# Kernel optimization log

Measured on AMD Instinct MI355X. Metric: run time of the kernel, lower is better.

Reference implementation:

```python
import jax, jax.numpy as jnp
import numpy as np

N_NODES = 50000
N_EDGES = 500000
N_GRAPHS = 256
D_IN, D_H1, D_H2, D_H3, D_OUT = 768, 256, 128, 64, 2


def _glorot(key, shape):
    fan_in, fan_out = shape[1], shape[0]
    lim = float(np.sqrt(6.0 / (fan_in + fan_out)))
    return jax.random.uniform(key, shape, jnp.float32, -lim, lim)


def setup_inputs() -> dict:
    key = jax.random.key(0)
    ks = jax.random.split(key, 12)
    x = jax.random.normal(ks[0], (N_NODES, D_IN), jnp.float32)
    edge_index = jax.random.randint(ks[1], (2, N_EDGES), 0, N_NODES, jnp.int64)
    batch = jnp.sort(jax.random.randint(ks[2], (N_NODES,), 0, N_GRAPHS, jnp.int64))
    return {
        "x": x,
        "edge_index": edge_index,
        "batch": batch,
        # SAGEConv1: out = lin_l(mean_aggr) + lin_r(x); bias only on lin_l (PyG default)
        "W1_l": _glorot(ks[3], (D_H1, D_IN)),
        "b1_l": jnp.zeros((D_H1,), jnp.float32),
        "W1_r": _glorot(ks[4], (D_H1, D_IN)),
        # SAGEConv2
        "W2_l": _glorot(ks[5], (D_H2, D_H1)),
        "b2_l": jnp.zeros((D_H2,), jnp.float32),
        "W2_r": _glorot(ks[6], (D_H2, D_H1)),
        # MLP head
        "W3": _glorot(ks[7], (D_H3, D_H2)),
        "b3": jnp.zeros((D_H3,), jnp.float32),
        "W4": _glorot(ks[8], (D_OUT, D_H3)),
        "b4": jnp.zeros((D_OUT,), jnp.float32),
    }


def _sage_conv(x, src, dst, deg_inv, W_l, b_l, W_r):
    # mean aggregation of neighbor features: scatter-add then divide by in-degree
    aggr = jax.ops.segment_sum(x[src], dst, num_segments=N_NODES)  # [N, d]
    aggr = aggr * deg_inv[:, None]
    return aggr @ W_l.T + b_l + x @ W_r.T


def reference(x, edge_index, batch, W1_l, b1_l, W1_r, W2_l, b2_l, W2_r, W3, b3, W4, b4):
    src, dst = edge_index[0], edge_index[1]
    deg = jax.ops.segment_sum(jnp.ones((N_EDGES,), x.dtype), dst, num_segments=N_NODES)
    deg_inv = jnp.where(deg > 0, 1.0 / jnp.maximum(deg, 1.0), 0.0)

    h = jax.nn.relu(_sage_conv(x, src, dst, deg_inv, W1_l, b1_l, W1_r))
    h = jax.nn.relu(_sage_conv(h, src, dst, deg_inv, W2_l, b2_l, W2_r))

    # global_mean_pool over graph ids
    pooled = jax.ops.segment_sum(h, batch, num_segments=N_GRAPHS)  # [G, 128]
    cnt = jax.ops.segment_sum(jnp.ones((N_NODES,), h.dtype), batch, num_segments=N_GRAPHS)
    pooled = pooled / jnp.maximum(cnt, 1.0)[:, None]

    # dropout is identity in eval mode
    h = pooled @ W3.T + b3
    h = h @ W4.T + b4
    return jax.nn.softmax(h, axis=-1)
```

## Files before the change

### kernel.cpp

```cpp
#include <hip/hip_runtime.h>
#include <cstdint>
#include <cstddef>

#define N_NODES 50000
#define N_EDGES 500000
#define N_GRAPHS 256
#define D_IN 768
#define D_H1 256
#define D_H2 128

typedef __attribute__((ext_vector_type(8))) __bf16 bf16x8;
typedef __attribute__((ext_vector_type(4))) float f32x4;

__device__ __forceinline__ float bf2f(uint32_t u) {
    union { uint32_t i; float f; } v; v.i = u << 16; return v.f;
}
__device__ __forceinline__ uint32_t f2bf(float f) {
    union { float f; uint32_t i; } v; v.f = f;
    uint32_t u = v.i;
    return (u + 0x7FFFu + ((u >> 16) & 1u)) >> 16;
}

#define HIST4_BLKS 489
#define PACKA4_BLKS 4688
#define PACKW1_BLKS 192
#define PACKW2_BLKS 32
#define NCHUNK_A 4800000
__global__ __launch_bounds__(256) void k_pack_hist(
    const float* __restrict__ x, uint16_t* __restrict__ xp,
    const float* __restrict__ W1l, const float* __restrict__ W1r, uint16_t* __restrict__ W1p,
    const float* __restrict__ W2l, const float* __restrict__ W2r, uint16_t* __restrict__ W2p,
    const int* __restrict__ e_dst, int* __restrict__ deg)
{
    int b = blockIdx.x, t = threadIdx.x;
    if (b < HIST4_BLKS) {
        int base = b * 1024 + t;
        #pragma unroll
        for (int j = 0; j < 4; ++j) {
            int e = base + j * 256;
            if (e < N_EDGES) atomicAdd(&deg[e_dst[e]], 1);
        }
    } else if (b < HIST4_BLKS + PACKA4_BLKS) {
        int c0 = (b - HIST4_BLKS) * 1024 + t;
        float4 u[4], v[4];
        #pragma unroll
        for (int j = 0; j < 4; ++j) {
            int c = c0 + j * 256; if (c > NCHUNK_A - 1) c = NCHUNK_A - 1;
            int l = c & 63, tt = c >> 6;
            int kt = tt % 24, mt = tt / 24;
            const float* p = x + (size_t)(mt * 16 + (l & 15)) * 768 + kt * 32 + (l >> 4) * 8;
            u[j] = *(const float4*)p;
            v[j] = *(const float4*)(p + 4);
        }
        #pragma unroll
        for (int j = 0; j < 4; ++j) {
            int c = c0 + j * 256; if (c > NCHUNK_A - 1) c = NCHUNK_A - 1;
            uint4 o;
            o.x = f2bf(u[j].x) | (f2bf(u[j].y) << 16);
            o.y = f2bf(u[j].z) | (f2bf(u[j].w) << 16);
            o.z = f2bf(v[j].x) | (f2bf(v[j].y) << 16);
            o.w = f2bf(v[j].z) | (f2bf(v[j].w) << 16);
            *(uint4*)(xp + (size_t)c * 8) = o;
        }
    } else if (b < HIST4_BLKS + PACKA4_BLKS + PACKW1_BLKS) {
        int c = (b - HIST4_BLKS - PACKA4_BLKS) * 256 + t;
        int l = c & 63, tt = c >> 6;
        int kt = tt % 24, mt = tt / 24;
        int row = mt * 16 + (l & 15);
        const float* src = (row < 256) ? (W1l + (size_t)row * 768)
                                       : (W1r + (size_t)(row - 256) * 768);
        const float* p = src + kt * 32 + (l >> 4) * 8;
        float4 u = *(const float4*)p, v = *(const float4*)(p + 4);
        uint4 o;
        o.x = f2bf(u.x) | (f2bf(u.y) << 16);
        o.y = f2bf(u.z) | (f2bf(u.w) << 16);
        o.z = f2bf(v.x) | (f2bf(v.y) << 16);
        o.w = f2bf(v.z) | (f2bf(v.w) << 16);
        *(uint4*)(W1p + (size_t)c * 8) = o;
    } else {
        int c = (b - HIST4_BLKS - PACKA4_BLKS - PACKW1_BLKS) * 256 + t;
        int l = c & 63, tt = c >> 6;
        int kt = tt % 8, mt = tt / 8;
        int row = mt * 16 + (l & 15);
        const float* src = (row < 128) ? (W2l + (size_t)row * 256)
                                       : (W2r + (size_t)(row - 128) * 256);
        const float* p = src + kt * 32 + (l >> 4) * 8;
        float4 u = *(const float4*)p, v = *(const float4*)(p + 4);
        uint4 o;
        o.x = f2bf(u.x) | (f2bf(u.y) << 16);
        o.y = f2bf(u.z) | (f2bf(u.w) << 16);
        o.z = f2bf(v.x) | (f2bf(v.y) << 16);
        o.w = f2bf(v.z) | (f2bf(v.w) << 16);
        *(uint4*)(W2p + (size_t)c * 8) = o;
    }
}

#define SCAN_BLKS 196
#define G1_OFF  SCAN_BLKS
#define G1_BLKS 784
#define FILL_OFF (G1_OFF + G1_BLKS)
#define FILL_BLKS 1954
__global__ __launch_bounds__(256, 2) void k_scan_gemm1_fill(
    const uint16_t* __restrict__ Ap, const uint16_t* __restrict__ Bp,
    uint16_t* __restrict__ Cl, uint16_t* __restrict__ Cr,
    const int* __restrict__ e_src, const int* __restrict__ e_dst,
    const int* __restrict__ deg, int* __restrict__ row_start,
    int* __restrict__ cursor, float* __restrict__ deg_inv,
    int* __restrict__ bsum, int* __restrict__ scan_done,
    int* __restrict__ csr_src)
{
    int t = threadIdx.x;
    if (blockIdx.x < SCAN_BLKS) {
        __shared__ int buf[256];
        __shared__ int bbuf[256];
        int b = blockIdx.x, i = b * 256 + t;
        int v = (i < N_NODES) ? deg[i] : 0;
        buf[t] = v; __syncthreads();
        for (int off = 1; off < 256; off <<= 1) {
            int u = (t >= off) ? buf[t - off] : 0;
            __syncthreads(); buf[t] += u; __syncthreads();
        }
        if (t == 255) atomicExch(&bsum[b], buf[255] + 1);
        int w = 0;
        if (t < SCAN_BLKS) {
            do { w = atomicAdd(&bsum[t], 0); } while (w == 0);
            w -= 1;
        }
        bbuf[t] = w; __syncthreads();
        for (int off = 1; off < 256; off <<= 1) {
            int u = (t >= off) ? bbuf[t - off] : 0;
            __syncthreads(); bbuf[t] += u; __syncthreads();
        }
        int base = (b > 0) ? bbuf[b - 1] : 0;
        if (i < N_NODES) {
            int rs = base + buf[t] - v;
            row_start[i] = rs;
            cursor[i] = rs;
            deg_inv[i] = (v > 0) ? (1.0f / (float)v) : 0.0f;
        }
        if (b == 0 && t == 0) row_start[N_NODES] = N_EDGES;
        __threadfence();
        __syncthreads();
        if (t == 0)
            __hip_atomic_fetch_add(scan_done, 1, __ATOMIC_RELEASE, __HIP_MEMORY_SCOPE_AGENT);
        return;
    }
    if (blockIdx.x >= FILL_OFF) {
        if (t < 64) {
            while (__hip_atomic_load(scan_done, __ATOMIC_ACQUIRE,
                                     __HIP_MEMORY_SCOPE_AGENT) < SCAN_BLKS)
                __builtin_amdgcn_s_sleep(8);
        }
        __syncthreads();
        int e = (blockIdx.x - FILL_OFF) * 256 + t;
        if (e < N_EDGES) {
            int d = e_dst[e];
            int pos = atomicAdd(&cursor[d], 1);
            csr_src[pos] = e_src[e];
        }
        return;
    }
    const int i = blockIdx.x - G1_OFF;
    const int pr = (i >> 4) * 8 + (i & 7);
    const int half = (i >> 3) & 1;
    if (pr >= 391) return;
    const int KT = 24;
    const int wave = t >> 6, lane = t & 63;
    const int fr = lane & 15, fq = lane >> 4;
    const int bm = pr * 128;
    const int wm = (wave >> 1) * 64, wn = (wave & 1) * 128;
    const int mtiles = (N_NODES + 15) >> 4;

    const bf16x8* ap[4];
    const bf16x8* bp[8];
    #pragma unroll
    for (int mi = 0; mi < 4; ++mi) {
        int mt = ((bm + wm) >> 4) + mi;
        if (mt > mtiles - 1) mt = mtiles - 1;
        ap[mi] = (const bf16x8*)Ap + (size_t)mt * KT * 64 + lane;
    }
    #pragma unroll
    for (int ni = 0; ni < 8; ++ni) {
        int nt = ((half * 256 + wn) >> 4) + ni;
        bp[ni] = (const bf16x8*)Bp + (size_t)nt * KT * 64 + lane;
    }

    f32x4 acc[4][8] = {};
    bf16x8 a0[4], b0[8], a1[4], b1[8];

    auto lA = [&](int kt, bf16x8* d) {
        #pragma unroll
        for (int mi = 0; mi < 4; ++mi) d[mi] = ap[mi][kt * 64];
    };
    auto lB = [&](int kt, bf16x8* d) {
        #pragma unroll
        for (int ni = 0; ni < 8; ++ni) d[ni] = bp[ni][kt * 64];
    };
    auto step = [&](bf16x8* a, bf16x8* b) {
        #pragma unroll
        for (int mi = 0; mi < 4; ++mi)
            #pragma unroll
            for (int ni = 0; ni < 8; ++ni)
                acc[mi][ni] = __builtin_amdgcn_mfma_f32_16x16x32_bf16(
                    a[mi], b[ni], acc[mi][ni], 0, 0, 0);
    };

    lA(0, a0); lB(0, b0);
    for (int ks = 0; ks < KT; ks += 2) {
        lA(ks + 1, a1); lB(ks + 1, b1);
        step(a0, b0);
        if (ks + 2 < KT) { lA(ks + 2, a0); lB(ks + 2, b0); }
        step(a1, b1);
    }

    uint16_t* __restrict__ C = half ? Cr : Cl;
    #pragma unroll
    for (int mi = 0; mi < 4; ++mi) {
        #pragma unroll
        for (int r = 0; r < 4; ++r) {
            int row = bm + wm + mi * 16 + fq * 4 + r;
            if (row >= N_NODES) continue;
            #pragma unroll
            for (int ni = 0; ni < 8; ++ni) {
                int col = wn + ni * 16 + fr;
                C[(size_t)row * 256 + col] = (uint16_t)f2bf(acc[mi][ni][r]);
            }
        }
    }
}

__global__ __launch_bounds__(256, 2) void k_mgemm(
    const uint16_t* __restrict__ Ap, const uint16_t* __restrict__ Bp,
    uint16_t* __restrict__ C, int M, int N, int KT)
{
    const int tid = threadIdx.x;
    const int wave = tid >> 6, lane = tid & 63;
    const int fr = lane & 15, fq = lane >> 4;
    const int bn = blockIdx.x * 256, bm = blockIdx.y * 128;
    const int wm = (wave >> 1) * 64, wn = (wave & 1) * 128;
    const int mtiles = (M + 15) >> 4;

    const bf16x8* ap[4];
    const bf16x8* bp[8];
    #pragma unroll
    for (int mi = 0; mi < 4; ++mi) {
        int mt = ((bm + wm) >> 4) + mi;
        if (mt > mtiles - 1) mt = mtiles - 1;
        ap[mi] = (const bf16x8*)Ap + (size_t)mt * KT * 64 + lane;
    }
    #pragma unroll
    for (int ni = 0; ni < 8; ++ni) {
        int nt = ((bn + wn) >> 4) + ni;
        bp[ni] = (const bf16x8*)Bp + (size_t)nt * KT * 64 + lane;
    }

    f32x4 acc[4][8] = {};
    bf16x8 a0[4], b0[8], a1[4], b1[8];

    auto lA = [&](int kt, bf16x8* d) {
        #pragma unroll
        for (int mi = 0; mi < 4; ++mi) d[mi] = ap[mi][kt * 64];
    };
    auto lB = [&](int kt, bf16x8* d) {
        #pragma unroll
        for (int ni = 0; ni < 8; ++ni) d[ni] = bp[ni][kt * 64];
    };
    auto step = [&](bf16x8* a, bf16x8* b) {
        #pragma unroll
        for (int mi = 0; mi < 4; ++mi)
            #pragma unroll
            for (int ni = 0; ni < 8; ++ni)
                acc[mi][ni] = __builtin_amdgcn_mfma_f32_16x16x32_bf16(
                    a[mi], b[ni], acc[mi][ni], 0, 0, 0);
    };

    lA(0, a0); lB(0, b0);
    for (int ks = 0; ks < KT; ks += 2) {
        lA(ks + 1, a1); lB(ks + 1, b1);
        step(a0, b0);
        if (ks + 2 < KT) { lA(ks + 2, a0); lB(ks + 2, b0); }
        step(a1, b1);
    }

    #pragma unroll
    for (int mi = 0; mi < 4; ++mi) {
        #pragma unroll
        for (int r = 0; r < 4; ++r) {
            int row = bm + wm + mi * 16 + fq * 4 + r;
            if (row >= M) continue;
            #pragma unroll
            for (int ni = 0; ni < 8; ++ni) {
                int col = bn + wn + ni * 16 + fr;
                C[(size_t)row * N + col] = (uint16_t)f2bf(acc[mi][ni][r]);
            }
        }
    }
}

__global__ __launch_bounds__(256) void k_agg1(
    const uint16_t* __restrict__ yl, const uint16_t* __restrict__ yr,
    const int* __restrict__ row_start, const int* __restrict__ csr,
    const float* __restrict__ deg_inv, const float* __restrict__ bias,
    uint16_t* __restrict__ h1p)
{
    int node = blockIdx.x * 8 + (threadIdx.x >> 5);
    if (node >= N_NODES) return;
    int c = threadIdx.x & 31;
    int s = row_start[node], e = row_start[node + 1];
    float a[8] = {};
    int p = s;
    auto accum = [&](uint4 t0) {
        a[0] += bf2f(t0.x & 0xFFFF); a[1] += bf2f(t0.x >> 16);
        a[2] += bf2f(t0.y & 0xFFFF); a[3] += bf2f(t0.y >> 16);
        a[4] += bf2f(t0.z & 0xFFFF); a[5] += bf2f(t0.z >> 16);
        a[6] += bf2f(t0.w & 0xFFFF); a[7] += bf2f(t0.w >> 16);
    };
    for (; p + 3 < e; p += 4) {
        uint4 t0 = *(const uint4*)(yl + (size_t)csr[p]     * 256 + c * 8);
        uint4 t1 = *(const uint4*)(yl + (size_t)csr[p + 1] * 256 + c * 8);
        uint4 t2 = *(const uint4*)(yl + (size_t)csr[p + 2] * 256 + c * 8);
        uint4 t3 = *(const uint4*)(yl + (size_t)csr[p + 3] * 256 + c * 8);
        accum(t0); accum(t1); accum(t2); accum(t3);
    }
    for (; p < e; ++p)
        accum(*(const uint4*)(yl + (size_t)csr[p] * 256 + c * 8));
    float w = deg_inv[node];
    uint4 tx = *(const uint4*)(yr + (size_t)node * 256 + c * 8);
    float4 b0 = *(const float4*)(bias + c * 8);
    float4 b1 = *(const float4*)(bias + c * 8 + 4);
    float v0 = fmaxf(a[0] * w + bf2f(tx.x & 0xFFFF) + b0.x, 0.f);
    float v1 = fmaxf(a[1] * w + bf2f(tx.x >> 16)    + b0.y, 0.f);
    float v2 = fmaxf(a[2] * w + bf2f(tx.y & 0xFFFF) + b0.z, 0.f);
    float v3 = fmaxf(a[3] * w + bf2f(tx.y >> 16)    + b0.w, 0.f);
    float v4 = fmaxf(a[4] * w + bf2f(tx.z & 0xFFFF) + b1.x, 0.f);
    float v5 = fmaxf(a[5] * w + bf2f(tx.z >> 16)    + b1.y, 0.f);
    float v6 = fmaxf(a[6] * w + bf2f(tx.w & 0xFFFF) + b1.z, 0.f);
    float v7 = fmaxf(a[7] * w + bf2f(tx.w >> 16)    + b1.w, 0.f);
    uint4 o;
    o.x = f2bf(v0) | (f2bf(v1) << 16);
    o.y = f2bf(v2) | (f2bf(v3) << 16);
    o.z = f2bf(v4) | (f2bf(v5) << 16);
    o.w = f2bf(v6) | (f2bf(v7) << 16);
    uint32_t addr = (((node >> 4) * 8 + (c >> 2)) * 64 + (c & 3) * 16 + (node & 15));
    *(uint4*)(h1p + (size_t)addr * 8) = o;
}

__global__ __launch_bounds__(256) void k_agg2(
    const uint16_t* __restrict__ y, const int* __restrict__ row_start,
    const int* __restrict__ csr, const float* __restrict__ deg_inv,
    const float* __restrict__ bias, float* __restrict__ out)
{
    int node = blockIdx.x * 4 + (threadIdx.x >> 6);
    if (node >= N_NODES) return;
    int lane = threadIdx.x & 63;
    int s = row_start[node], e = row_start[node + 1];
    float a0 = 0.f, a1 = 0.f;
    int p = s;
    for (; p + 3 < e; p += 4) {
        uint32_t t0 = *(const uint32_t*)(y + (size_t)csr[p]     * 256 + lane * 2);
        uint32_t t1 = *(const uint32_t*)(y + (size_t)csr[p + 1] * 256 + lane * 2);
        uint32_t t2 = *(const uint32_t*)(y + (size_t)csr[p + 2] * 256 + lane * 2);
        uint32_t t3 = *(const uint32_t*)(y + (size_t)csr[p + 3] * 256 + lane * 2);
        a0 += bf2f(t0 & 0xFFFF) + bf2f(t1 & 0xFFFF) + bf2f(t2 & 0xFFFF) + bf2f(t3 & 0xFFFF);
        a1 += bf2f(t0 >> 16)    + bf2f(t1 >> 16)    + bf2f(t2 >> 16)    + bf2f(t3 >> 16);
    }
    for (; p < e; ++p) {
        uint32_t t0 = *(const uint32_t*)(y + (size_t)csr[p] * 256 + lane * 2);
        a0 += bf2f(t0 & 0xFFFF);
        a1 += bf2f(t0 >> 16);
    }
    float w = deg_inv[node];
    uint32_t tx = *(const uint32_t*)(y + (size_t)node * 256 + 128 + lane * 2);
    float2 b = *(const float2*)(bias + lane * 2);
    float2 o;
    o.x = fmaxf(a0 * w + bf2f(tx & 0xFFFF) + b.x, 0.f);
    o.y = fmaxf(a1 * w + bf2f(tx >> 16)    + b.y, 0.f);
    *(float2*)(out + (size_t)node * 128 + lane * 2) = o;
}

__global__ void k_poolhead(const float* __restrict__ h2, const int* __restrict__ batch,
                           const float* __restrict__ W3, const float* __restrict__ b3,
                           const float* __restrict__ W4, const float* __restrict__ b4,
                           float* __restrict__ out)
{
    int g = blockIdx.x;
    __shared__ int s_lo, s_hi;
    __shared__ float p[128];
    __shared__ float hid[64];
    __shared__ float logit[2];
    int t = threadIdx.x;
    if (t == 0) {
        int lo = 0, hi = N_NODES;
        while (lo < hi) { int m = (lo + hi) >> 1; if (batch[m] < g) lo = m + 1; else hi = m; }
        s_lo = lo;
        int lo2 = lo, hi2 = N_NODES;
        while (lo2 < hi2) { int m = (lo2 + hi2) >> 1; if (batch[m] < g + 1) lo2 = m + 1; else hi2 = m; }
        s_hi = lo2;
    }
    __syncthreads();
    float sum = 0.f;
    for (int i = s_lo; i < s_hi; ++i) sum += h2[(size_t)i * D_H2 + t];
    int cnt = s_hi - s_lo;
    p[t] = sum / (float)(cnt > 0 ? cnt : 1);
    __syncthreads();
    if (t < 64) {
        float s = b3[t];
        #pragma unroll 4
        for (int k = 0; k < 128; ++k) s = fmaf(p[k], W3[t * 128 + k], s);
        hid[t] = s;
    }
    __syncthreads();
    if (t < 2) {
        float l = b4[t];
        for (int k = 0; k < 64; ++k) l = fmaf(hid[k], W4[t * 64 + k], l);
        logit[t] = l;
    }
    __syncthreads();
    if (t == 0) {
        float m = fmaxf(logit[0], logit[1]);
        float e0 = expf(logit[0] - m), e1 = expf(logit[1] - m);
        float inv = 1.0f / (e0 + e1);
        out[g * 2 + 0] = e0 * inv;
        out[g * 2 + 1] = e1 * inv;
    }
}

extern "C" void kernel_launch(void* const* d_in, const int* in_sizes, int n_in,
                              void* d_out, int out_size, void* d_ws, size_t ws_size,
                              hipStream_t stream)
{
    const float* x     = (const float*)d_in[0];
    const int*   ei    = (const int*)d_in[1];
    const int*   batch = (const int*)d_in[2];
    const float* W1l   = (const float*)d_in[3];
    const float* b1l   = (const float*)d_in[4];
    const float* W1r   = (const float*)d_in[5];
    const float* W2l   = (const float*)d_in[6];
    const float* b2l   = (const float*)d_in[7];
    const float* W2r   = (const float*)d_in[8];
    const float* W3    = (const float*)d_in[9];
    const float* b3    = (const float*)d_in[10];
    const float* W4    = (const float*)d_in[11];
    const float* b4    = (const float*)d_in[12];
    float* out = (float*)d_out;

    const int* e_src = ei;
    const int* e_dst = ei + N_EDGES;

    char* ws = (char*)d_ws;
    size_t off = 0;
    auto alloc = [&](size_t bytes) -> void* {
        void* p = ws + off;
        off = (off + bytes + 255) & ~(size_t)255;
        return p;
    };
    int*      deg       = (int*)alloc((size_t)(N_NODES + 256 + 64) * 4);
    int*      bsum      = deg + N_NODES;
    int*      scan_done = bsum + 256;
    int*      row_start = (int*)alloc((size_t)(N_NODES + 1) * 4);
    int*      cursor    = (int*)alloc((size_t)N_NODES * 4);
    int*      csr_src   = (int*)alloc((size_t)N_EDGES * 4);
    float*    deg_inv   = (float*)alloc((size_t)N_NODES * 4);
    uint16_t* W1p       = (uint16_t*)alloc((size_t)512 * 768 * 2);
    uint16_t* W2p       = (uint16_t*)alloc((size_t)256 * 256 * 2);
    uint16_t* xp        = (uint16_t*)alloc((size_t)N_NODES * D_IN * 2);
    uint16_t* y1        = (uint16_t*)alloc((size_t)N_NODES * 512 * 2);
    uint16_t* h1p       = (uint16_t*)alloc((size_t)N_NODES * 256 * 2);

    uint16_t* y1l = y1;
    uint16_t* y1r = y1 + (size_t)N_NODES * 256;
    uint16_t* y2 = xp;
    float*    h2 = (float*)(xp + (size_t)N_NODES * 256);

    hipMemsetAsync(deg, 0, (size_t)(N_NODES + 256 + 64) * 4, stream);

    k_pack_hist<<<HIST4_BLKS + PACKA4_BLKS + PACKW1_BLKS + PACKW2_BLKS, 256, 0, stream>>>(
        x, xp, W1l, W1r, W1p, W2l, W2r, W2p, e_dst, deg);

    k_scan_gemm1_fill<<<FILL_OFF + FILL_BLKS, 256, 0, stream>>>(
        xp, W1p, y1l, y1r, e_src, e_dst, deg, row_start, cursor, deg_inv,
        bsum, scan_done, csr_src);
    k_agg1<<<(N_NODES + 7) / 8, 256, 0, stream>>>(y1l, y1r, row_start, csr_src, deg_inv, b1l, h1p);

    dim3 g2(1, (N_NODES + 127) / 128);
    k_mgemm<<<g2, 256, 0, stream>>>(h1p, W2p, y2, N_NODES, 256, 8);
    k_agg2<<<(N_NODES + 3) / 4, 256, 0, stream>>>(y2, row_start, csr_src, deg_inv, b2l, h2);

    k_poolhead<<<N_GRAPHS, 128, 0, stream>>>(h2, batch, W3, b3, W4, b4, out);
}
```

Baseline: 503.9 us.

## Split scan into separate kernel and shrink GEMM1 tiles to 64-row slabs

Moves the degree prefix scan out of the fused GEMM1/fill kernel into its own launch, so the fill blocks no longer spin-wait on a global counter. GEMM1 tiles go from 128x256 per block to 64x256, with each wave computing a 64x64 tile, which doubles the block count (1568) for better occupancy and load balance. Each block now reuses its A tile across fewer output columns and adds an extra kernel launch, and the scan can no longer overlap with GEMM1.

```diff
diff --git a/kernel.cpp b/kernel.cpp
--- a/kernel.cpp
+++ b/kernel.cpp
@@ -95,64 +95,53 @@
     }
 }
 
-#define SCAN_BLKS 196
-#define G1_OFF  SCAN_BLKS
-#define G1_BLKS 784
-#define FILL_OFF (G1_OFF + G1_BLKS)
+__global__ __launch_bounds__(256) void k_scan(
+    const int* __restrict__ deg, int* __restrict__ row_start, int* __restrict__ cursor,
+    float* __restrict__ deg_inv, int* __restrict__ bsum, int n, int nb)
+{
+    __shared__ int buf[256];
+    __shared__ int bbuf[256];
+    int t = threadIdx.x, b = blockIdx.x, i = b * 256 + t;
+    int v = (i < n) ? deg[i] : 0;
+    buf[t] = v; __syncthreads();
+    for (int off = 1; off < 256; off <<= 1) {
+        int u = (t >= off) ? buf[t - off] : 0;
+        __syncthreads(); buf[t] += u; __syncthreads();
+    }
+    if (t == 255) atomicExch(&bsum[b], buf[255] + 1);
+    int w = 0;
+    if (t < nb) {
+        do { w = atomicAdd(&bsum[t], 0); } while (w == 0);
+        w -= 1;
+    }
+    bbuf[t] = w; __syncthreads();
+    for (int off = 1; off < 256; off <<= 1) {
+        int u = (t >= off) ? bbuf[t - off] : 0;
+        __syncthreads(); bbuf[t] += u; __syncthreads();
+    }
+    int base = (b > 0) ? bbuf[b - 1] : 0;
+    if (i < n) {
+        int rs = base + buf[t] - v;
+        row_start[i] = rs;
+        cursor[i] = rs;
+        deg_inv[i] = (v > 0) ? (1.0f / (float)v) : 0.0f;
+    }
+    if (b == 0 && t == 0) row_start[n] = N_EDGES;
+}
+
+#define NSLAB 782
+#define G1_GROUPS 98
+#define G1_BLKS (G1_GROUPS * 16)
 #define FILL_BLKS 1954
-__global__ __launch_bounds__(256, 2) void k_scan_gemm1_fill(
+__global__ __launch_bounds__(256, 2) void k_gemm1_fill(
     const uint16_t* __restrict__ Ap, const uint16_t* __restrict__ Bp,
     uint16_t* __restrict__ Cl, uint16_t* __restrict__ Cr,
     const int* __restrict__ e_src, const int* __restrict__ e_dst,
-    const int* __restrict__ deg, int* __restrict__ row_start,
-    int* __restrict__ cursor, float* __restrict__ deg_inv,
-    int* __restrict__ bsum, int* __restrict__ scan_done,
-    int* __restrict__ csr_src)
+    int* __restrict__ cursor, int* __restrict__ csr_src)
 {
     int t = threadIdx.x;
-    if (blockIdx.x < SCAN_BLKS) {
-        __shared__ int buf[256];
-        __shared__ int bbuf[256];
-        int b = blockIdx.x, i = b * 256 + t;
-        int v = (i < N_NODES) ? deg[i] : 0;
-        buf[t] = v; __syncthreads();
-        for (int off = 1; off < 256; off <<= 1) {
-            int u = (t >= off) ? buf[t - off] : 0;
-            __syncthreads(); buf[t] += u; __syncthreads();
-        }
-        if (t == 255) atomicExch(&bsum[b], buf[255] + 1);
-        int w = 0;
-        if (t < SCAN_BLKS) {
-            do { w = atomicAdd(&bsum[t], 0); } while (w == 0);
-            w -= 1;
-        }
-        bbuf[t] = w; __syncthreads();
-        for (int off = 1; off < 256; off <<= 1) {
-            int u = (t >= off) ? bbuf[t - off] : 0;
-            __syncthreads(); bbuf[t] += u; __syncthreads();
-        }
-        int base = (b > 0) ? bbuf[b - 1] : 0;
-        if (i < N_NODES) {
-            int rs = base + buf[t] - v;
-            row_start[i] = rs;
-            cursor[i] = rs;
-            deg_inv[i] = (v > 0) ? (1.0f / (float)v) : 0.0f;
-        }
-        if (b == 0 && t == 0) row_start[N_NODES] = N_EDGES;
-        __threadfence();
-        __syncthreads();
-        if (t == 0)
-            __hip_atomic_fetch_add(scan_done, 1, __ATOMIC_RELEASE, __HIP_MEMORY_SCOPE_AGENT);
-        return;
-    }
-    if (blockIdx.x >= FILL_OFF) {
-        if (t < 64) {
-            while (__hip_atomic_load(scan_done, __ATOMIC_ACQUIRE,
-                                     __HIP_MEMORY_SCOPE_AGENT) < SCAN_BLKS)
-                __builtin_amdgcn_s_sleep(8);
-        }
-        __syncthreads();
-        int e = (blockIdx.x - FILL_OFF) * 256 + t;
+    if (blockIdx.x >= G1_BLKS) {
+        int e = (blockIdx.x - G1_BLKS) * 256 + t;
         if (e < N_EDGES) {
             int d = e_dst[e];
             int pos = atomicAdd(&cursor[d], 1);
@@ -160,33 +149,32 @@
         }
         return;
     }
-    const int i = blockIdx.x - G1_OFF;
+    const int i = blockIdx.x;
     const int pr = (i >> 4) * 8 + (i & 7);
     const int half = (i >> 3) & 1;
-    if (pr >= 391) return;
+    if (pr >= NSLAB) return;
     const int KT = 24;
     const int wave = t >> 6, lane = t & 63;
     const int fr = lane & 15, fq = lane >> 4;
-    const int bm = pr * 128;
-    const int wm = (wave >> 1) * 64, wn = (wave & 1) * 128;
+    const int bm = pr * 64;
     const int mtiles = (N_NODES + 15) >> 4;
 
     const bf16x8* ap[4];
-    const bf16x8* bp[8];
+    const bf16x8* bp[4];
     #pragma unroll
     for (int mi = 0; mi < 4; ++mi) {
-        int mt = ((bm + wm) >> 4) + mi;
+        int mt = (bm >> 4) + mi;
         if (mt > mtiles - 1) mt = mtiles - 1;
         ap[mi] = (const bf16x8*)Ap + (size_t)mt * KT * 64 + lane;
     }
     #pragma unroll
-    for (int ni = 0; ni < 8; ++ni) {
-        int nt = ((half * 256 + wn) >> 4) + ni;
+    for (int ni = 0; ni < 4; ++ni) {
+        int nt = half * 16 + wave * 4 + ni;
         bp[ni] = (const bf16x8*)Bp + (size_t)nt * KT * 64 + lane;
     }
 
-    f32x4 acc[4][8] = {};
-    bf16x8 a0[4], b0[8], a1[4], b1[8];
+    f32x4 acc[4][4] = {};
+    bf16x8 a0[4], b0[4], a1[4], b1[4];
 
     auto lA = [&](int kt, bf16x8* d) {
         #pragma unroll
@@ -194,13 +182,13 @@
     };
     auto lB = [&](int kt, bf16x8* d) {
         #pragma unroll
-        for (int ni = 0; ni < 8; ++ni) d[ni] = bp[ni][kt * 64];
+        for (int ni = 0; ni < 4; ++ni) d[ni] = bp[ni][kt * 64];
     };
     auto step = [&](bf16x8* a, bf16x8* b) {
         #pragma unroll
         for (int mi = 0; mi < 4; ++mi)
             #pragma unroll
-            for (int ni = 0; ni < 8; ++ni)
+            for (int ni = 0; ni < 4; ++ni)
                 acc[mi][ni] = __builtin_amdgcn_mfma_f32_16x16x32_bf16(
                     a[mi], b[ni], acc[mi][ni], 0, 0, 0);
     };
@@ -218,11 +206,11 @@
     for (int mi = 0; mi < 4; ++mi) {
         #pragma unroll
         for (int r = 0; r < 4; ++r) {
-            int row = bm + wm + mi * 16 + fq * 4 + r;
+            int row = bm + mi * 16 + fq * 4 + r;
             if (row >= N_NODES) continue;
             #pragma unroll
-            for (int ni = 0; ni < 8; ++ni) {
-                int col = wn + ni * 16 + fr;
+            for (int ni = 0; ni < 4; ++ni) {
+                int col = wave * 64 + ni * 16 + fr;
                 C[(size_t)row * 256 + col] = (uint16_t)f2bf(acc[mi][ni][r]);
             }
         }
@@ -454,9 +442,8 @@
         off = (off + bytes + 255) & ~(size_t)255;
         return p;
     };
-    int*      deg       = (int*)alloc((size_t)(N_NODES + 256 + 64) * 4);
+    int*      deg       = (int*)alloc((size_t)(N_NODES + 256) * 4);
     int*      bsum      = deg + N_NODES;
-    int*      scan_done = bsum + 256;
     int*      row_start = (int*)alloc((size_t)(N_NODES + 1) * 4);
     int*      cursor    = (int*)alloc((size_t)N_NODES * 4);
     int*      csr_src   = (int*)alloc((size_t)N_EDGES * 4);
@@ -472,14 +459,16 @@
     uint16_t* y2 = xp;
     float*    h2 = (float*)(xp + (size_t)N_NODES * 256);
 
-    hipMemsetAsync(deg, 0, (size_t)(N_NODES + 256 + 64) * 4, stream);
+    hipMemsetAsync(deg, 0, (size_t)(N_NODES + 256) * 4, stream);
 
     k_pack_hist<<<HIST4_BLKS + PACKA4_BLKS + PACKW1_BLKS + PACKW2_BLKS, 256, 0, stream>>>(
         x, xp, W1l, W1r, W1p, W2l, W2r, W2p, e_dst, deg);
 
-    k_scan_gemm1_fill<<<FILL_OFF + FILL_BLKS, 256, 0, stream>>>(
-        xp, W1p, y1l, y1r, e_src, e_dst, deg, row_start, cursor, deg_inv,
-        bsum, scan_done, csr_src);
+    int nscan = (N_NODES + 255) / 256;
+    k_scan<<<nscan, 256, 0, stream>>>(deg, row_start, cursor, deg_inv, bsum, N_NODES, nscan);
+
+    k_gemm1_fill<<<G1_BLKS + FILL_BLKS, 256, 0, stream>>>(
+        xp, W1p, y1l, y1r, e_src, e_dst, cursor, csr_src);
     k_agg1<<<(N_NODES + 7) / 8, 256, 0, stream>>>(y1l, y1r, row_start, csr_src, deg_inv, b1l, h1p);
 
     dim3 g2(1, (N_NODES + 127) / 128);
```

After: 489.1 us. 2.9% less time.
